# Performance work log

Hardware: AMD Instinct MI355X
Metric: run time of the kernel (lower is better)

## Reference

```python
import jax, jax.numpy as jnp
import numpy as np

B, C, H, W = 4, 256, 64, 64
CQ = C // 8


def setup_inputs() -> dict:
    key = jax.random.key(0)
    ks = jax.random.split(key, 8)
    s = 0.02
    return {
        "x": jax.random.normal(ks[0], (B, C, H, W), dtype=jnp.float32),
        "Wq": jax.random.normal(ks[1], (CQ, C), dtype=jnp.float32) * s,
        "bq": jax.random.normal(ks[2], (CQ,), dtype=jnp.float32) * s,
        "Wk": jax.random.normal(ks[3], (CQ, C), dtype=jnp.float32) * s,
        "bk": jax.random.normal(ks[4], (CQ,), dtype=jnp.float32) * s,
        "Wv": jax.random.normal(ks[5], (C, C), dtype=jnp.float32) * s,
        "bv": jax.random.normal(ks[6], (C,), dtype=jnp.float32) * s,
        "gamma": jax.random.normal(ks[7], (1,), dtype=jnp.float32) * s,
    }


def reference(x, Wq, bq, Wk, bk, Wv, bv, gamma):
    b, c, h, w = x.shape
    n = h * w
    xf = x.reshape(b, c, n)  # [B,C,N]; 1x1 conv == channel matmul
    q = jnp.einsum("oc,bcn->bno", Wq, xf) + bq  # [B,N,CQ]
    k = jnp.einsum("oc,bcn->bon", Wk, xf) + bk[:, None]  # [B,CQ,N]
    v = jnp.einsum("oc,bcn->bno", Wv, xf) + bv  # [B,N,C]
    attn = jnp.einsum("bnd,bdm->bnm", q, k)  # [B,N,N], unscaled
    attn = jax.nn.softmax(attn, axis=1)  # non-standard axis (over rows)
    out = jnp.einsum("bnm,bmc->bnc", attn, v)  # [B,N,C]
    out = out.transpose(0, 2, 1).reshape(b, c, h, w)
    return gamma * out + x
```

## Files before the change

kernel.cpp:

```cpp
#include <hip/hip_runtime.h>

#define B_ 4
#define C_ 256
#define N_ 4096
#define LOG2E 1.44269504088896340736f

typedef __attribute__((ext_vector_type(8))) short bf16x8;
typedef __attribute__((ext_vector_type(4))) float f32x4;

static __device__ __forceinline__ unsigned short f2bf(float f) {
    unsigned u = __builtin_bit_cast(unsigned, f);
    u += 0x7fffu + ((u >> 16) & 1u);
    return (unsigned short)(u >> 16);
}

static __device__ __forceinline__ float fexp2(float x) {
#if __has_builtin(__builtin_amdgcn_exp2f)
    return __builtin_amdgcn_exp2f(x);
#else
    return exp2f(x);
#endif
}

#define LDS_BARRIER() asm volatile("s_waitcnt lgkmcnt(0)\n\ts_barrier" ::: "memory")

__global__ void k0_wprep(const float* __restrict__ Wq, const float* __restrict__ Wk,
                         const float* __restrict__ Wv, float* __restrict__ WqkT,
                         unsigned short* __restrict__ wvb) {
    int t = blockIdx.x * 256 + threadIdx.x;
    if (t < 256 * 64) {
        int c = t >> 6, o = t & 63;
        WqkT[t] = (o < 32) ? Wq[o * C_ + c] * LOG2E : Wk[(o - 32) * C_ + c];
    }
    int t2 = t - 256 * 64;
    if (t2 >= 0 && t2 < 256 * 256) wvb[t2] = f2bf(Wv[t2]);
}

__global__ __launch_bounds__(256) void k1_qkx(const float* __restrict__ x,
        const float* __restrict__ WqkT, const float* __restrict__ bq,
        const float* __restrict__ bk, unsigned short* __restrict__ qb,
        unsigned short* __restrict__ ktb, unsigned short* __restrict__ xb) {
    __shared__ float red[4][64][64];
    int b = blockIdx.y;
    int n0 = blockIdx.x * 64;
    int l = threadIdx.x & 63, v = threadIdx.x >> 6;
    const float* xp = x + (size_t)b * C_ * N_ + n0 + l;
    unsigned short* xbp = xb + (size_t)b * C_ * N_ + n0 + l;
    float acc[64];
#pragma unroll
    for (int o = 0; o < 64; ++o) acc[o] = 0.0f;
    for (int c = 64 * v; c < 64 * v + 64; ++c) {
        float xv = xp[(size_t)c * N_];
        xbp[(size_t)c * N_] = f2bf(xv);
        const float4* wr4 = (const float4*)(WqkT + c * 64);
#pragma unroll
        for (int o4 = 0; o4 < 16; ++o4) {
            float4 wv = wr4[o4];
            acc[4 * o4 + 0] += wv.x * xv;
            acc[4 * o4 + 1] += wv.y * xv;
            acc[4 * o4 + 2] += wv.z * xv;
            acc[4 * o4 + 3] += wv.w * xv;
        }
    }
#pragma unroll
    for (int o = 0; o < 64; ++o) red[v][l][o] = acc[o];
    __syncthreads();
    int n = threadIdx.x & 63, og = threadIdx.x >> 6;
    int o0 = og * 16;
    unsigned pk[8];
#pragma unroll
    for (int i = 0; i < 8; ++i) {
        int oa = o0 + 2 * i, ob = oa + 1;
        float va = red[0][n][oa] + red[1][n][oa] + red[2][n][oa] + red[3][n][oa];
        float vb = red[0][n][ob] + red[1][n][ob] + red[2][n][ob] + red[3][n][ob];
        if (og < 2) { va += bq[oa] * LOG2E; vb += bq[ob] * LOG2E; }
        else        { va += bk[oa - 32];    vb += bk[ob - 32]; }
        pk[i] = (unsigned)f2bf(va) | ((unsigned)f2bf(vb) << 16);
    }
    unsigned short* dst = (og < 2)
        ? qb + ((size_t)b * N_ + n0 + n) * 32 + o0
        : ktb + ((size_t)b * N_ + n0 + n) * 32 + (o0 - 32);
    ((uint4*)dst)[0] = make_uint4(pk[0], pk[1], pk[2], pk[3]);
    ((uint4*)dst)[1] = make_uint4(pk[4], pk[5], pk[6], pk[7]);
}

__global__ __launch_bounds__(512) void k2_stats(const unsigned short* __restrict__ qb,
        const unsigned short* __restrict__ ktb, float* __restrict__ Wcol) {
    __shared__ float red[64][33];
    int b = blockIdx.y;
    int m0 = blockIdx.x * 64;
    int lane = threadIdx.x & 63, w = threadIdx.x >> 6;
    int r16 = lane & 15, g = lane >> 4;
    const unsigned short* kb = ktb + ((size_t)b * N_ + m0 + r16) * 32 + 8 * g;
    bf16x8 kf0 = *(const bf16x8*)(kb);
    bf16x8 kf1 = *(const bf16x8*)(kb + 16 * 32);
    bf16x8 kf2 = *(const bf16x8*)(kb + 32 * 32);
    bf16x8 kf3 = *(const bf16x8*)(kb + 48 * 32);
    float z0 = 0, z1 = 0, z2 = 0, z3 = 0;
    const unsigned short* qbase = qb + ((size_t)b * N_ + w * 512 + r16) * 32 + 8 * g;
#pragma unroll 2
    for (int n0 = 0; n0 < 512; n0 += 16) {
        bf16x8 qf = *(const bf16x8*)(qbase + (size_t)n0 * 32);
        f32x4 d0 = __builtin_amdgcn_mfma_f32_16x16x32_bf16(qf, kf0, (f32x4){0, 0, 0, 0}, 0, 0, 0);
        f32x4 d1 = __builtin_amdgcn_mfma_f32_16x16x32_bf16(qf, kf1, (f32x4){0, 0, 0, 0}, 0, 0, 0);
        f32x4 d2 = __builtin_amdgcn_mfma_f32_16x16x32_bf16(qf, kf2, (f32x4){0, 0, 0, 0}, 0, 0, 0);
        f32x4 d3 = __builtin_amdgcn_mfma_f32_16x16x32_bf16(qf, kf3, (f32x4){0, 0, 0, 0}, 0, 0, 0);
        z0 += fexp2(d0[0]) + fexp2(d0[1]) + fexp2(d0[2]) + fexp2(d0[3]);
        z1 += fexp2(d1[0]) + fexp2(d1[1]) + fexp2(d1[2]) + fexp2(d1[3]);
        z2 += fexp2(d2[0]) + fexp2(d2[1]) + fexp2(d2[2]) + fexp2(d2[3]);
        z3 += fexp2(d3[0]) + fexp2(d3[1]) + fexp2(d3[2]) + fexp2(d3[3]);
    }
    red[r16][4 * w + g] = z0;
    red[16 + r16][4 * w + g] = z1;
    red[32 + r16][4 * w + g] = z2;
    red[48 + r16][4 * w + g] = z3;
    __syncthreads();
    if (threadIdx.x < 64) {
        float s = 0;
#pragma unroll
        for (int i = 0; i < 32; ++i) s += red[threadIdx.x][i];
        Wcol[(size_t)b * N_ + m0 + threadIdx.x] = 1.0f / s;
    }
}

__global__ __launch_bounds__(512) void k4_y(const unsigned short* __restrict__ qb,
        const unsigned short* __restrict__ ktb, const unsigned short* __restrict__ xb,
        const float* __restrict__ Wcol, unsigned short* __restrict__ Yt,
        float* __restrict__ rowP) {
    __shared__ unsigned short Pl[3][64 * 64];
    __shared__ float rpl[4][64];
    int b = blockIdx.y;
    int n0 = blockIdx.x * 64;
    int lane = threadIdx.x & 63, w = threadIdx.x >> 6;
    int ms = w >> 1, wn = w & 1;
    int r16 = lane & 15, g = lane >> 4;
    int swz = (r16 & 7) << 4;

    const unsigned short* qbp = qb + ((size_t)b * N_ + n0 + 32 * wn + r16) * 32 + 8 * g;
    bf16x8 qf0 = *(const bf16x8*)(qbp);
    bf16x8 qf1 = *(const bf16x8*)(qbp + 16 * 32);
    const unsigned short* kbp = ktb + ((size_t)b * N_ + 16 * ms + r16) * 32 + 8 * g;
    const unsigned short* xbp = xb + ((size_t)b * C_ + 32 * w + r16) * N_ + 8 * g;
    const float* izp = Wcol + (size_t)b * N_ + 16 * ms + 4 * g;

    char* pwbase = (char*)&Pl[0][0] + (32 * wn + r16) * 128 + ((32 * ms + 8 * g) ^ swz);

    f32x4 acc[4][2];
#pragma unroll
    for (int i = 0; i < 4; ++i)
#pragma unroll
        for (int j = 0; j < 2; ++j) acc[i][j] = (f32x4){0, 0, 0, 0};
    float rp0 = 0.0f, rp1 = 0.0f;

#define S_STEP(KAV, IZV, WJ)                                                          \
    {                                                                                 \
        f32x4 s0 = __builtin_amdgcn_mfma_f32_16x16x32_bf16(KAV, qf0, (f32x4){0,0,0,0}, 0, 0, 0); \
        f32x4 s1 = __builtin_amdgcn_mfma_f32_16x16x32_bf16(KAV, qf1, (f32x4){0,0,0,0}, 0, 0, 0); \
        float p00 = fexp2(s0[0]) * IZV.x, p01 = fexp2(s0[1]) * IZV.y;                 \
        float p02 = fexp2(s0[2]) * IZV.z, p03 = fexp2(s0[3]) * IZV.w;                 \
        float p10 = fexp2(s1[0]) * IZV.x, p11 = fexp2(s1[1]) * IZV.y;                 \
        float p12 = fexp2(s1[2]) * IZV.z, p13 = fexp2(s1[3]) * IZV.w;                 \
        rp0 += p00 + p01 + p02 + p03;                                                 \
        rp1 += p10 + p11 + p12 + p13;                                                 \
        char* pw = pwbase + (WJ) * 8192;                                              \
        *(uint2*)(pw) = make_uint2(                                                   \
            (unsigned)f2bf(p00) | ((unsigned)f2bf(p01) << 16),                        \
            (unsigned)f2bf(p02) | ((unsigned)f2bf(p03) << 16));                       \
        *(uint2*)(pw + 16 * 128) = make_uint2(                                        \
            (unsigned)f2bf(p10) | ((unsigned)f2bf(p11) << 16),                        \
            (unsigned)f2bf(p12) | ((unsigned)f2bf(p13) << 16));                       \
    }

    bf16x8 kt0 = *(const bf16x8*)(kbp);
    bf16x8 kt1 = *(const bf16x8*)(kbp + (size_t)64 * 32);
    float4 it0 = *(const float4*)(izp);
    float4 it1 = *(const float4*)(izp + 64);
    bf16x8 kq0 = *(const bf16x8*)(kbp + (size_t)128 * 32);
    bf16x8 kq1 = *(const bf16x8*)(kbp + (size_t)192 * 32);
    bf16x8 kq2 = *(const bf16x8*)(kbp + (size_t)256 * 32);
    float4 izq0 = *(const float4*)(izp + 128);
    float4 izq1 = *(const float4*)(izp + 192);
    float4 izq2 = *(const float4*)(izp + 256);
    bf16x8 xq0[2][2], xq1[2][2], xq2[2][2];
#pragma unroll
    for (int cs = 0; cs < 2; ++cs)
#pragma unroll
        for (int ks = 0; ks < 2; ++ks) {
            xq0[cs][ks] = *(const bf16x8*)(xbp + (size_t)cs * 16 * N_ + 32 * ks);
            xq1[cs][ks] = *(const bf16x8*)(xbp + (size_t)cs * 16 * N_ + 64 + 32 * ks);
            xq2[cs][ks] = *(const bf16x8*)(xbp + (size_t)cs * 16 * N_ + 128 + 32 * ks);
        }
    S_STEP(kt0, it0, 0);
    S_STEP(kt1, it1, 1);
    LDS_BARRIER();

#define BODY(T, J, WJ)                                                                \
    {                                                                                 \
        const char* prd = (const char*)&Pl[(J)][0] + r16 * 128;                       \
        bf16x8 pa[4][2];                                                              \
        _Pragma("unroll") for (int ns = 0; ns < 4; ++ns)                              \
            _Pragma("unroll") for (int ks = 0; ks < 2; ++ks)                          \
                pa[ns][ks] = *(const bf16x8*)(prd + ns * 16 * 128 +                   \
                                              ((64 * ks + 16 * g) ^ swz));            \
        if ((T) < 62) S_STEP(kq##J, izq##J, WJ);                                      \
        _Pragma("unroll") for (int ns = 0; ns < 4; ++ns)                              \
            _Pragma("unroll") for (int cs = 0; cs < 2; ++cs)                          \
                _Pragma("unroll") for (int ks = 0; ks < 2; ++ks)                      \
                    acc[ns][cs] = __builtin_amdgcn_mfma_f32_16x16x32_bf16(            \
                        pa[ns][ks], xq##J[cs][ks], acc[ns][cs], 0, 0, 0);             \
        kq##J = *(const bf16x8*)(kbp + (size_t)((T) + 5) * 64 * 32);                  \
        izq##J = *(const float4*)(izp + (size_t)((T) + 5) * 64);                      \
        _Pragma("unroll") for (int cs = 0; cs < 2; ++cs)                              \
            _Pragma("unroll") for (int ks = 0; ks < 2; ++ks)                          \
                xq##J[cs][ks] = *(const bf16x8*)(xbp + (size_t)cs * 16 * N_ +         \
                                                 (size_t)((T) + 3) * 64 + 32 * ks);   \
        LDS_BARRIER();                                                                \
    }

    for (int u = 0; u < 21; ++u) {
        int t0 = 3 * u;
        BODY(t0, 0, 2);
        BODY(t0 + 1, 1, 0);
        BODY(t0 + 2, 2, 1);
    }
    {
        const char* prd = (const char*)&Pl[0][0] + r16 * 128;
        bf16x8 pa[4][2];
#pragma unroll
        for (int ns = 0; ns < 4; ++ns)
#pragma unroll
            for (int ks = 0; ks < 2; ++ks)
                pa[ns][ks] = *(const bf16x8*)(prd + ns * 16 * 128 + ((64 * ks + 16 * g) ^ swz));
#pragma unroll
        for (int ns = 0; ns < 4; ++ns)
#pragma unroll
            for (int cs = 0; cs < 2; ++cs)
#pragma unroll
                for (int ks = 0; ks < 2; ++ks)
                    acc[ns][cs] = __builtin_amdgcn_mfma_f32_16x16x32_bf16(
                        pa[ns][ks], xq0[cs][ks], acc[ns][cs], 0, 0, 0);
    }
#undef BODY
#undef S_STEP

    rp0 += __shfl_xor(rp0, 16); rp0 += __shfl_xor(rp0, 32);
    rp1 += __shfl_xor(rp1, 16); rp1 += __shfl_xor(rp1, 32);
    if (g == 0) {
        rpl[ms][32 * wn + r16] = rp0;
        rpl[ms][32 * wn + 16 + r16] = rp1;
    }
    __syncthreads();
    if (threadIdx.x < 64)
        rowP[(size_t)b * N_ + n0 + threadIdx.x] =
            rpl[0][threadIdx.x] + rpl[1][threadIdx.x] + rpl[2][threadIdx.x] + rpl[3][threadIdx.x];

#pragma unroll
    for (int ns = 0; ns < 4; ++ns)
#pragma unroll
        for (int cs = 0; cs < 2; ++cs) {
            int cp = 32 * w + 16 * cs + r16;
            f32x4 a = acc[ns][cs];
#pragma unroll
            for (int r = 0; r < 4; ++r) {
                int n = n0 + 16 * ns + 4 * g + r;
                Yt[((size_t)b * N_ + n) * C_ + cp] = f2bf(a[r]);
            }
        }
}

__global__ __launch_bounds__(256) void k5_out(const float* __restrict__ x,
        const unsigned short* __restrict__ wvb, const unsigned short* __restrict__ Yt,
        const float* __restrict__ rowP, const float* __restrict__ bv,
        const float* __restrict__ gamma, float* __restrict__ out) {
    int b = blockIdx.y;
    int n0 = blockIdx.x * 32;
    int lane = threadIdx.x & 63, w = threadIdx.x >> 6;
    int r16 = lane & 15, g = lane >> 4;
    const unsigned short* wvp = wvb + (64 * w + r16) * C_ + 8 * g;
    const unsigned short* ytp = Yt + ((size_t)b * N_ + n0 + r16) * C_ + 8 * g;

    f32x4 acc[4][2];
#pragma unroll
    for (int i = 0; i < 4; ++i)
#pragma unroll
        for (int j = 0; j < 2; ++j) acc[i][j] = (f32x4){0, 0, 0, 0};

#pragma unroll
    for (int kc = 0; kc < 8; ++kc) {
        bf16x8 yf[2];
#pragma unroll
        for (int ns = 0; ns < 2; ++ns)
            yf[ns] = *(const bf16x8*)(ytp + ns * 16 * C_ + kc * 32);
#pragma unroll
        for (int cs = 0; cs < 4; ++cs) {
            bf16x8 wf = *(const bf16x8*)(wvp + cs * 16 * C_ + kc * 32);
#pragma unroll
            for (int ns = 0; ns < 2; ++ns)
                acc[cs][ns] = __builtin_amdgcn_mfma_f32_16x16x32_bf16(
                    wf, yf[ns], acc[cs][ns], 0, 0, 0);
        }
    }
    float gm = gamma[0];
    float rpv[2];
#pragma unroll
    for (int ns = 0; ns < 2; ++ns) rpv[ns] = rowP[(size_t)b * N_ + n0 + 16 * ns + r16];
#pragma unroll
    for (int cs = 0; cs < 4; ++cs) {
        float4 bvv = *(const float4*)(bv + 64 * w + 16 * cs + 4 * g);
        float bva[4] = {bvv.x, bvv.y, bvv.z, bvv.w};
#pragma unroll
        for (int ns = 0; ns < 2; ++ns)
#pragma unroll
            for (int r = 0; r < 4; ++r) {
                int c = 64 * w + 16 * cs + 4 * g + r;
                int n = n0 + 16 * ns + r16;
                size_t idx = ((size_t)b * C_ + c) * N_ + n;
                out[idx] = gm * (acc[cs][ns][r] + rpv[ns] * bva[r]) + x[idx];
            }
    }
}

extern "C" void kernel_launch(void* const* d_in, const int* in_sizes, int n_in,
                              void* d_out, int out_size, void* d_ws, size_t ws_size,
                              hipStream_t stream) {
    const float* x = (const float*)d_in[0];
    const float* Wq = (const float*)d_in[1];
    const float* bq = (const float*)d_in[2];
    const float* Wk = (const float*)d_in[3];
    const float* bk = (const float*)d_in[4];
    const float* Wv = (const float*)d_in[5];
    const float* bv = (const float*)d_in[6];
    const float* gamma = (const float*)d_in[7];
    float* out = (float*)d_out;

    char* ws = (char*)d_ws;
    unsigned short* qb  = (unsigned short*)(ws);
    unsigned short* ktb = (unsigned short*)(ws + (1u << 20));
    unsigned short* xb  = (unsigned short*)(ws + (2u << 20));
    unsigned short* Yt  = (unsigned short*)(ws + (10u << 20));
    float* Wcol = (float*)(ws + (18u << 20));
    float* WqkT = (float*)(ws + (18u << 20) + (1u << 16));
    unsigned short* wvb = (unsigned short*)(ws + (18u << 20) + (2u << 16));
    float* rowP = (float*)(ws + (18u << 20) + (4u << 16));

    k0_wprep<<<320, 256, 0, stream>>>(Wq, Wk, Wv, WqkT, wvb);
    k1_qkx<<<dim3(N_ / 64, B_), 256, 0, stream>>>(x, WqkT, bq, bk, qb, ktb, xb);
    k2_stats<<<dim3(N_ / 64, B_), 512, 0, stream>>>(qb, ktb, Wcol);
    k4_y<<<dim3(N_ / 64, B_), 512, 0, stream>>>(qb, ktb, xb, Wcol, Yt, rowP);
    k5_out<<<dim3(N_ / 32, B_), 256, 0, stream>>>(x, wvb, Yt, rowP, bv, gamma, out);
}
```

Before: 228.4 us.

## Split k4_y channel dimension across blocks with 4-wave blocks

k4_y changes from 8 waves per block covering all 256 channels to 4 waves per block, with a grid z dimension of 2 that splits the output channels into halves. Each wave now computes scores for all 64 query rows (four MFMAs per step) over its own 16-column slice. This doubles the block count to raise occupancy and parallelism, but the QK^T score and exp work is recomputed once per channel half. k1 also marks the wave index as uniform with readfirstlane.

```diff
diff --git a/kernel.cpp b/kernel.cpp
--- a/kernel.cpp
+++ b/kernel.cpp
@@ -43,7 +43,8 @@
     __shared__ float red[4][64][64];
     int b = blockIdx.y;
     int n0 = blockIdx.x * 64;
-    int l = threadIdx.x & 63, v = threadIdx.x >> 6;
+    int l = threadIdx.x & 63;
+    int v = __builtin_amdgcn_readfirstlane((int)(threadIdx.x >> 6));
     const float* xp = x + (size_t)b * C_ * N_ + n0 + l;
     unsigned short* xbp = xb + (size_t)b * C_ * N_ + n0 + l;
     float acc[64];
@@ -123,7 +124,7 @@
     }
 }
 
-__global__ __launch_bounds__(512) void k4_y(const unsigned short* __restrict__ qb,
+__global__ __launch_bounds__(256) void k4_y(const unsigned short* __restrict__ qb,
         const unsigned short* __restrict__ ktb, const unsigned short* __restrict__ xb,
         const float* __restrict__ Wcol, unsigned short* __restrict__ Yt,
         float* __restrict__ rowP) {
@@ -131,44 +132,60 @@
     __shared__ float rpl[4][64];
     int b = blockIdx.y;
     int n0 = blockIdx.x * 64;
+    int ch = blockIdx.z;
     int lane = threadIdx.x & 63, w = threadIdx.x >> 6;
-    int ms = w >> 1, wn = w & 1;
     int r16 = lane & 15, g = lane >> 4;
     int swz = (r16 & 7) << 4;
 
-    const unsigned short* qbp = qb + ((size_t)b * N_ + n0 + 32 * wn + r16) * 32 + 8 * g;
+    const unsigned short* qbp = qb + ((size_t)b * N_ + n0 + r16) * 32 + 8 * g;
     bf16x8 qf0 = *(const bf16x8*)(qbp);
     bf16x8 qf1 = *(const bf16x8*)(qbp + 16 * 32);
-    const unsigned short* kbp = ktb + ((size_t)b * N_ + 16 * ms + r16) * 32 + 8 * g;
-    const unsigned short* xbp = xb + ((size_t)b * C_ + 32 * w + r16) * N_ + 8 * g;
-    const float* izp = Wcol + (size_t)b * N_ + 16 * ms + 4 * g;
-
-    char* pwbase = (char*)&Pl[0][0] + (32 * wn + r16) * 128 + ((32 * ms + 8 * g) ^ swz);
+    bf16x8 qf2 = *(const bf16x8*)(qbp + 32 * 32);
+    bf16x8 qf3 = *(const bf16x8*)(qbp + 48 * 32);
+    const unsigned short* kbp = ktb + ((size_t)b * N_ + 16 * w + r16) * 32 + 8 * g;
+    const unsigned short* xbp = xb + ((size_t)b * C_ + 128 * ch + 32 * w + r16) * N_ + 8 * g;
+    const float* izp = Wcol + (size_t)b * N_ + 16 * w + 4 * g;
+
+    char* pwbase = (char*)&Pl[0][0] + r16 * 128 + ((32 * w + 8 * g) ^ swz);
 
     f32x4 acc[4][2];
 #pragma unroll
     for (int i = 0; i < 4; ++i)
 #pragma unroll
         for (int j = 0; j < 2; ++j) acc[i][j] = (f32x4){0, 0, 0, 0};
-    float rp0 = 0.0f, rp1 = 0.0f;
+    float rp0 = 0.0f, rp1 = 0.0f, rp2 = 0.0f, rp3 = 0.0f;
 
 #define S_STEP(KAV, IZV, WJ)                                                          \
     {                                                                                 \
         f32x4 s0 = __builtin_amdgcn_mfma_f32_16x16x32_bf16(KAV, qf0, (f32x4){0,0,0,0}, 0, 0, 0); \
         f32x4 s1 = __builtin_amdgcn_mfma_f32_16x16x32_bf16(KAV, qf1, (f32x4){0,0,0,0}, 0, 0, 0); \
-        float p00 = fexp2(s0[0]) * IZV.x, p01 = fexp2(s0[1]) * IZV.y;                 \
-        float p02 = fexp2(s0[2]) * IZV.z, p03 = fexp2(s0[3]) * IZV.w;                 \
-        float p10 = fexp2(s1[0]) * IZV.x, p11 = fexp2(s1[1]) * IZV.y;                 \
-        float p12 = fexp2(s1[2]) * IZV.z, p13 = fexp2(s1[3]) * IZV.w;                 \
-        rp0 += p00 + p01 + p02 + p03;                                                 \
-        rp1 += p10 + p11 + p12 + p13;                                                 \
+        f32x4 s2 = __builtin_amdgcn_mfma_f32_16x16x32_bf16(KAV, qf2, (f32x4){0,0,0,0}, 0, 0, 0); \
+        f32x4 s3 = __builtin_amdgcn_mfma_f32_16x16x32_bf16(KAV, qf3, (f32x4){0,0,0,0}, 0, 0, 0); \
         char* pw = pwbase + (WJ) * 8192;                                              \
+        float pa0 = fexp2(s0[0]) * IZV.x, pa1 = fexp2(s0[1]) * IZV.y;                 \
+        float pa2 = fexp2(s0[2]) * IZV.z, pa3 = fexp2(s0[3]) * IZV.w;                 \
+        rp0 += pa0 + pa1 + pa2 + pa3;                                                 \
         *(uint2*)(pw) = make_uint2(                                                   \
-            (unsigned)f2bf(p00) | ((unsigned)f2bf(p01) << 16),                        \
-            (unsigned)f2bf(p02) | ((unsigned)f2bf(p03) << 16));                       \
+            (unsigned)f2bf(pa0) | ((unsigned)f2bf(pa1) << 16),                        \
+            (unsigned)f2bf(pa2) | ((unsigned)f2bf(pa3) << 16));                       \
+        float pb0 = fexp2(s1[0]) * IZV.x, pb1 = fexp2(s1[1]) * IZV.y;                 \
+        float pb2 = fexp2(s1[2]) * IZV.z, pb3 = fexp2(s1[3]) * IZV.w;                 \
+        rp1 += pb0 + pb1 + pb2 + pb3;                                                 \
         *(uint2*)(pw + 16 * 128) = make_uint2(                                        \
-            (unsigned)f2bf(p10) | ((unsigned)f2bf(p11) << 16),                        \
-            (unsigned)f2bf(p12) | ((unsigned)f2bf(p13) << 16));                       \
+            (unsigned)f2bf(pb0) | ((unsigned)f2bf(pb1) << 16),                        \
+            (unsigned)f2bf(pb2) | ((unsigned)f2bf(pb3) << 16));                       \
+        float pc0 = fexp2(s2[0]) * IZV.x, pc1 = fexp2(s2[1]) * IZV.y;                 \
+        float pc2 = fexp2(s2[2]) * IZV.z, pc3 = fexp2(s2[3]) * IZV.w;                 \
+        rp2 += pc0 + pc1 + pc2 + pc3;                                                 \
+        *(uint2*)(pw + 32 * 128) = make_uint2(                                        \
+            (unsigned)f2bf(pc0) | ((unsigned)f2bf(pc1) << 16),                        \
+            (unsigned)f2bf(pc2) | ((unsigned)f2bf(pc3) << 16));                       \
+        float pd0 = fexp2(s3[0]) * IZV.x, pd1 = fexp2(s3[1]) * IZV.y;                 \
+        float pd2 = fexp2(s3[2]) * IZV.z, pd3 = fexp2(s3[3]) * IZV.w;                 \
+        rp3 += pd0 + pd1 + pd2 + pd3;                                                 \
+        *(uint2*)(pw + 48 * 128) = make_uint2(                                        \
+            (unsigned)f2bf(pd0) | ((unsigned)f2bf(pd1) << 16),                        \
+            (unsigned)f2bf(pd2) | ((unsigned)f2bf(pd3) << 16));                       \
     }
 
     bf16x8 kt0 = *(const bf16x8*)(kbp);
@@ -245,12 +262,16 @@
 
     rp0 += __shfl_xor(rp0, 16); rp0 += __shfl_xor(rp0, 32);
     rp1 += __shfl_xor(rp1, 16); rp1 += __shfl_xor(rp1, 32);
+    rp2 += __shfl_xor(rp2, 16); rp2 += __shfl_xor(rp2, 32);
+    rp3 += __shfl_xor(rp3, 16); rp3 += __shfl_xor(rp3, 32);
     if (g == 0) {
-        rpl[ms][32 * wn + r16] = rp0;
-        rpl[ms][32 * wn + 16 + r16] = rp1;
+        rpl[w][r16] = rp0;
+        rpl[w][16 + r16] = rp1;
+        rpl[w][32 + r16] = rp2;
+        rpl[w][48 + r16] = rp3;
     }
     __syncthreads();
-    if (threadIdx.x < 64)
+    if (ch == 0 && threadIdx.x < 64)
         rowP[(size_t)b * N_ + n0 + threadIdx.x] =
             rpl[0][threadIdx.x] + rpl[1][threadIdx.x] + rpl[2][threadIdx.x] + rpl[3][threadIdx.x];
 
@@ -258,7 +279,7 @@
     for (int ns = 0; ns < 4; ++ns)
 #pragma unroll
         for (int cs = 0; cs < 2; ++cs) {
-            int cp = 32 * w + 16 * cs + r16;
+            int cp = 128 * ch + 32 * w + 16 * cs + r16;
             f32x4 a = acc[ns][cs];
 #pragma unroll
             for (int r = 0; r < 4; ++r) {
@@ -346,6 +367,6 @@
     k0_wprep<<<320, 256, 0, stream>>>(Wq, Wk, Wv, WqkT, wvb);
     k1_qkx<<<dim3(N_ / 64, B_), 256, 0, stream>>>(x, WqkT, bq, bk, qb, ktb, xb);
     k2_stats<<<dim3(N_ / 64, B_), 512, 0, stream>>>(qb, ktb, Wcol);
-    k4_y<<<dim3(N_ / 64, B_), 512, 0, stream>>>(qb, ktb, xb, Wcol, Yt, rowP);
+    k4_y<<<dim3(N_ / 64, B_, 2), 256, 0, stream>>>(qb, ktb, xb, Wcol, Yt, rowP);
     k5_out<<<dim3(N_ / 32, B_), 256, 0, stream>>>(x, wvb, Yt, rowP, bv, gamma, out);
 }
```

New measurement: 233.1 us. 2.1% more time.
